# Optimization experiments

Measured on AMD Instinct MI355X. Metric: run time of the kernel, lower is better.

## Reference

```python
import jax, jax.numpy as jnp
import numpy as np

B, C, L, K = 64, 2, 131072, 4


def setup_inputs() -> dict:
    key = jax.random.key(0)
    k1, k2, k3, k4 = jax.random.split(key, 4)
    x = jax.random.normal(k1, (B, C, L), dtype=jnp.float32)
    Bs = 0.5 * jax.random.normal(k2, (B, C, K, 3), dtype=jnp.float32)
    # Build stable denominators: complex-conjugate poles r*exp(+-j*theta), r < 0.95
    # a(z) = 1 - 2 r cos(theta) z^-1 + r^2 z^-2  -> guaranteed-stable IIR cascade.
    r = jax.random.uniform(k3, (B, C, K), minval=0.1, maxval=0.95)
    theta = jax.random.uniform(k4, (B, C, K), minval=0.05, maxval=np.pi - 0.05)
    a1 = -2.0 * r * jnp.cos(theta)
    a2 = r * r
    As = jnp.stack([jnp.ones_like(a1), a1, a2], axis=-1).astype(jnp.float32)
    return {"input_signal": x, "Bs": Bs, "As": As}


def _biquad_cascade(x, b, a):
    # x: [N, L]; b, a: [N, K, 3] with a already normalized (a0 == 1).
    # Serial cascade of K biquads, each in direct form II transposed:
    #   y[n]  = b0*u[n] + s1
    #   s1'   = b1*u[n] - a1*y[n] + s2
    #   s2'   = b2*u[n] - a2*y[n]
    # Exactly the linear recurrence the ssm/lfilter backends compute.
    nK = b.shape[1]
    b0, b1, b2 = b[..., 0], b[..., 1], b[..., 2]  # each [N, K]
    a1, a2 = a[..., 1], a[..., 2]

    def step(carry, xt):
        s1, s2 = carry  # each [N, K]
        u = xt  # [N]
        s1n, s2n = [], []
        for k in range(nK):  # small fixed cascade depth, unrolled
            y = b0[:, k] * u + s1[:, k]
            s1n.append(b1[:, k] * u - a1[:, k] * y + s2[:, k])
            s2n.append(b2[:, k] * u - a2[:, k] * y)
            u = y
        return (jnp.stack(s1n, axis=1), jnp.stack(s2n, axis=1)), u

    N = x.shape[0]
    init = (jnp.zeros((N, nK), x.dtype), jnp.zeros((N, nK), x.dtype))
    _, ys = jax.lax.scan(step, init, x.T)  # scan over time: ys [L, N]
    return ys.T


def reference(input_signal, Bs, As):
    b, c, audio_len = input_signal.shape
    assert Bs.shape[-1] == As.shape[-1] == 3
    # channel broadcasting as in _process_ssm
    if c == 1 and Bs.shape[1] > 1:
        input_signal = jnp.broadcast_to(input_signal, (b, Bs.shape[1], audio_len))
        c = Bs.shape[1]
    elif Bs.shape[1] == 1 and c > 1:
        Bs = jnp.broadcast_to(Bs, (b, c) + Bs.shape[2:])
        As = jnp.broadcast_to(As, (b, c) + As.shape[2:])
    a0 = As[..., :1]
    Bn = (Bs / a0).reshape(b * c, -1, 3)
    An = (As / a0).reshape(b * c, -1, 3)
    x = input_signal.reshape(b * c, audio_len)
    y = _biquad_cascade(x, Bn, An)
    return y.reshape(b, c, audio_len)
```

## Files before the change

kernel.cpp:

```cpp
#include <hip/hip_runtime.h>
#include <math.h>


#define SS   64
#define WMAX 384
#define WMIN 64
#define TT   32
#define TPB  256
#define LSTR 33
#define KB   4
#define NL   8

typedef float vf4 __attribute__((ext_vector_type(4)));

__global__ void iir_prep_kernel(const float* __restrict__ As, int rows,
                                int* __restrict__ wrow, int* __restrict__ perm)
{
    __shared__ int sw[256];
    const int r = threadIdx.x;
    int W = 0;
    if (r < rows) {
        float r2max = 0.f;
#pragma unroll
        for (int k = 0; k < KB; ++k) {
            float a0 = As[(size_t)r * KB * 3 + 3 * k];
            float a2 = As[(size_t)r * KB * 3 + 3 * k + 2] / a0;
            r2max = fmaxf(r2max, a2);
        }
        float rmax = fminf(fmaxf(sqrtf(fmaxf(r2max, 0.f)), 0.20f), 0.955f);
        float Wf = 25.6f / (-logf(rmax));
        W = ((int)ceilf(Wf) + TT - 1) & ~(TT - 1);
        W = min(max(W, WMIN), WMAX);
        wrow[r] = W;
    }
    sw[r] = W;
    __syncthreads();
    if (r < rows) {
        int rank = 0;
        for (int i = 0; i < rows; ++i)
            rank += (sw[i] > W) || (sw[i] == W && i < r);
        perm[rank] = r;
    }
}

__global__ __launch_bounds__(TPB, 4) void iir_chunks_kernel(
    const float* __restrict__ x, const float* __restrict__ Bs,
    const float* __restrict__ As, float* __restrict__ out, int L,
    const int* __restrict__ wrow, const int* __restrict__ perm)
{
    __shared__ float lds[TPB * LSTR];
    const int tid = threadIdx.x;
    const int bpr = (L / SS) / TPB;
    const int row = perm[blockIdx.x / bpr];
    const int chunk0 = (blockIdx.x % bpr) * TPB;
    const int W = wrow[row];

    float b0[KB], b1[KB], b2[KB], na1[KB], na2[KB];
    const float* Bp = Bs + (size_t)row * KB * 3;
    const float* Ap = As + (size_t)row * KB * 3;
#pragma unroll
    for (int k = 0; k < KB; ++k) {
        float inv = 1.0f / Ap[3 * k];
        b0[k]  =  Bp[3 * k]     * inv;
        b1[k]  =  Bp[3 * k + 1] * inv;
        b2[k]  =  Bp[3 * k + 2] * inv;
        na1[k] = -Ap[3 * k + 1] * inv;
        na2[k] = -Ap[3 * k + 2] * inv;
    }

    float s1[KB] = {0.f, 0.f, 0.f, 0.f};
    float s2[KB] = {0.f, 0.f, 0.f, 0.f};

    const float* xrow = x   + (size_t)row * L;
    float*       orow = out + (size_t)row * L;
    float*       myrow = lds + tid * LSTR;

    const int tq = tid >> 3;
    const int p4 = (tid & 7) << 2;
    int off[NL];
    int ldsoff[NL];
#pragma unroll
    for (int l = 0; l < NL; ++l) {
        int j = l * 32 + tq;
        off[l]    = (chunk0 + j) * SS + p4 - W;
        ldsoff[l] = j * LSTR + p4;
    }

    const int NT = (SS + W) / TT;
    const int WT = W / TT;

    float4 rn[NL];
#pragma unroll
    for (int l = 0; l < NL; ++l) {
        int pos = off[l];
        rn[l] = make_float4(0.f, 0.f, 0.f, 0.f);
        if (pos >= 0) rn[l] = *reinterpret_cast<const float4*>(xrow + pos);
    }

#pragma unroll 1
    for (int it = 0; it < NT; ++it) {
        __syncthreads();

#pragma unroll
        for (int l = 0; l < NL; ++l) {
            float* d = lds + ldsoff[l];
            d[0] = rn[l].x; d[1] = rn[l].y; d[2] = rn[l].z; d[3] = rn[l].w;
        }

        if (it + 1 < NT) {
            const int base = (it + 1) * TT;
#pragma unroll
            for (int l = 0; l < NL; ++l) {
                int pos = off[l] + base;
                rn[l] = make_float4(0.f, 0.f, 0.f, 0.f);
                if (pos >= 0) rn[l] = *reinterpret_cast<const float4*>(xrow + pos);
            }
        }

        __syncthreads();

        if (it < WT) {
#pragma unroll
            for (int p = 0; p < TT; ++p) {
                float u = myrow[p];
#pragma unroll
                for (int k = 0; k < KB; ++k) {
                    float yv = fmaf(b0[k], u, s1[k]);
                    s1[k] = fmaf(na1[k], yv, fmaf(b1[k], u, s2[k]));
                    s2[k] = fmaf(na2[k], yv, b2[k] * u);
                    u = yv;
                }
            }
        } else {
#pragma unroll
            for (int p = 0; p < TT; ++p) {
                float u = myrow[p];
#pragma unroll
                for (int k = 0; k < KB; ++k) {
                    float yv = fmaf(b0[k], u, s1[k]);
                    s1[k] = fmaf(na1[k], yv, fmaf(b1[k], u, s2[k]));
                    s2[k] = fmaf(na2[k], yv, b2[k] * u);
                    u = yv;
                }
                myrow[p] = u;
            }
            __syncthreads();

            const int base = it * TT - W;
#pragma unroll
            for (int l = 0; l < NL; ++l) {
                const float* sp = lds + ldsoff[l];
                vf4 v = { sp[0], sp[1], sp[2], sp[3] };
                __builtin_nontemporal_store(
                    v, reinterpret_cast<vf4*>(orow + off[l] + W + base));
            }
        }
    }
}

extern "C" void kernel_launch(void* const* d_in, const int* in_sizes, int n_in,
                              void* d_out, int out_size, void* d_ws, size_t ws_size,
                              hipStream_t stream) {
    const float* x  = (const float*)d_in[0];
    const float* Bs = (const float*)d_in[1];
    const float* As = (const float*)d_in[2];
    float* out = (float*)d_out;

    const int rows = in_sizes[1] / (KB * 3);
    const int L    = in_sizes[0] / rows;
    const int bpr  = (L / SS) / TPB;

    int* wrow = (int*)d_ws;
    int* perm = wrow + rows;

    hipLaunchKernelGGL(iir_prep_kernel, dim3(1), dim3(256), 0, stream,
                       As, rows, wrow, perm);
    hipLaunchKernelGGL(iir_chunks_kernel, dim3(rows * bpr), dim3(TPB), 0, stream,
                       x, Bs, As, out, L, wrow, perm);
}
```

Baseline: 141.2 us.

## Replace warm-up halo recompute with chunk-state pass plus transition-matrix combine

```diff
diff --git a/kernel.cpp b/kernel.cpp
--- a/kernel.cpp
+++ b/kernel.cpp
@@ -10,8 +10,311 @@
 #define LSTR 33
 #define KB   4
 #define NL   8
+#define HALO 6
+#define DSTR 9
 
 typedef float vf4 __attribute__((ext_vector_type(4)));
+
+__global__ void iir_prep2_kernel(const float* __restrict__ Bs,
+                                 const float* __restrict__ As, int rows,
+                                 int* __restrict__ nwrow,
+                                 float* __restrict__ nmat)
+{
+    __shared__ float mat[4][3][64];
+    const int grp  = threadIdx.x >> 6;
+    const int lane = threadIdx.x & 63;
+    const int row  = blockIdx.x * 4 + grp;
+    const bool act = (row < rows);
+
+    float b0[KB], b1[KB], b2[KB], na1[KB], na2[KB];
+    if (act) {
+        const float* Bp = Bs + (size_t)row * KB * 3;
+        const float* Ap = As + (size_t)row * KB * 3;
+#pragma unroll
+        for (int k = 0; k < KB; ++k) {
+            float inv = 1.0f / Ap[3 * k];
+            b0[k]  =  Bp[3 * k]     * inv;
+            b1[k]  =  Bp[3 * k + 1] * inv;
+            b2[k]  =  Bp[3 * k + 2] * inv;
+            na1[k] = -Ap[3 * k + 1] * inv;
+            na2[k] = -Ap[3 * k + 2] * inv;
+        }
+    }
+
+    float* cur = &mat[grp][0][0];
+    float* nxt = &mat[grp][1][0];
+    float* n1  = &mat[grp][2][0];
+
+    if (act && lane < 8) {
+        float s[8];
+#pragma unroll
+        for (int i = 0; i < 8; ++i) s[i] = (i == lane) ? 1.0f : 0.0f;
+        float u = 0.0f;
+#pragma unroll
+        for (int k = 0; k < KB; ++k) {
+            float y  = fmaf(b0[k], u, s[2 * k]);
+            float t1 = fmaf(na1[k], y, fmaf(b1[k], u, s[2 * k + 1]));
+            float t2 = fmaf(na2[k], y, b2[k] * u);
+            s[2 * k] = t1; s[2 * k + 1] = t2; u = y;
+        }
+#pragma unroll
+        for (int i = 0; i < 8; ++i) cur[i * 8 + lane] = s[i];
+    }
+    __syncthreads();
+
+    const int i8 = lane >> 3, j8 = lane & 7;
+
+    for (int t = 0; t < 6; ++t) {
+        float acc = 0.0f;
+        if (act) {
+#pragma unroll
+            for (int m = 0; m < 8; ++m)
+                acc = fmaf(cur[i8 * 8 + m], cur[m * 8 + j8], acc);
+            nxt[lane] = acc;
+        }
+        __syncthreads();
+        float* t0 = cur; cur = nxt; nxt = t0;
+    }
+
+    if (act) {
+        float v = cur[lane];
+        n1[lane] = v;
+        nmat[(size_t)row * 320 + lane] = v;
+    }
+    __syncthreads();
+
+    for (int m = 2; m <= 5; ++m) {
+        float acc = 0.0f;
+        if (act) {
+#pragma unroll
+            for (int q = 0; q < 8; ++q)
+                acc = fmaf(cur[i8 * 8 + q], n1[q * 8 + j8], acc);
+            nxt[lane] = acc;
+            nmat[(size_t)row * 320 + (m - 1) * 64 + lane] = acc;
+        }
+        __syncthreads();
+        float* t0 = cur; cur = nxt; nxt = t0;
+    }
+
+    if (act && lane == 0) {
+        const float* Ap = As + (size_t)row * KB * 3;
+        float r2max = 0.0f;
+#pragma unroll
+        for (int k = 0; k < KB; ++k) {
+            float a0 = Ap[3 * k];
+            float a2 = Ap[3 * k + 2] / a0;
+            r2max = fmaxf(r2max, a2);
+        }
+        float rmax = fminf(fmaxf(sqrtf(fmaxf(r2max, 0.f)), 0.20f), 0.955f);
+        float Wf = 25.6f / (-logf(rmax));
+        int W = ((int)ceilf(Wf) + TT - 1) & ~(TT - 1);
+        W = min(max(W, WMIN), WMAX);
+        nwrow[row] = (W + SS - 1) / SS;
+    }
+}
+
+__global__ __launch_bounds__(TPB, 4) void iir_state_kernel(
+    const float* __restrict__ x, const float* __restrict__ Bs,
+    const float* __restrict__ As, int L, float* __restrict__ dstate)
+{
+    __shared__ float lds[TPB * LSTR];
+    const int tid = threadIdx.x;
+    const int cpr = L / SS;
+    const int bpr = cpr / TPB;
+    const int row = blockIdx.x / bpr;
+    const int chunk0 = (blockIdx.x % bpr) * TPB;
+
+    float b0[KB], b1[KB], b2[KB], na1[KB], na2[KB];
+    const float* Bp = Bs + (size_t)row * KB * 3;
+    const float* Ap = As + (size_t)row * KB * 3;
+#pragma unroll
+    for (int k = 0; k < KB; ++k) {
+        float inv = 1.0f / Ap[3 * k];
+        b0[k]  =  Bp[3 * k]     * inv;
+        b1[k]  =  Bp[3 * k + 1] * inv;
+        b2[k]  =  Bp[3 * k + 2] * inv;
+        na1[k] = -Ap[3 * k + 1] * inv;
+        na2[k] = -Ap[3 * k + 2] * inv;
+    }
+
+    float s1[KB] = {0.f, 0.f, 0.f, 0.f};
+    float s2[KB] = {0.f, 0.f, 0.f, 0.f};
+
+    const float* xrow = x + (size_t)row * L;
+    float* myrow = lds + tid * LSTR;
+
+    const int tq = tid >> 3;
+    const int p4 = (tid & 7) << 2;
+    int off[NL], ldsoff[NL];
+#pragma unroll
+    for (int l = 0; l < NL; ++l) {
+        int j = l * 32 + tq;
+        off[l]    = (chunk0 + j) * SS + p4;
+        ldsoff[l] = j * LSTR + p4;
+    }
+
+    float4 rn[NL];
+#pragma unroll
+    for (int l = 0; l < NL; ++l)
+        rn[l] = *reinterpret_cast<const float4*>(xrow + off[l]);
+
+#pragma unroll
+    for (int it = 0; it < SS / TT; ++it) {
+        __syncthreads();
+#pragma unroll
+        for (int l = 0; l < NL; ++l) {
+            float* d = lds + ldsoff[l];
+            d[0] = rn[l].x; d[1] = rn[l].y; d[2] = rn[l].z; d[3] = rn[l].w;
+        }
+        if (it + 1 < SS / TT) {
+            const int base = (it + 1) * TT;
+#pragma unroll
+            for (int l = 0; l < NL; ++l)
+                rn[l] = *reinterpret_cast<const float4*>(xrow + off[l] + base);
+        }
+        __syncthreads();
+
+#pragma unroll
+        for (int p = 0; p < TT; ++p) {
+            float u = myrow[p];
+#pragma unroll
+            for (int k = 0; k < KB; ++k) {
+                float yv = fmaf(b0[k], u, s1[k]);
+                s1[k] = fmaf(na1[k], yv, fmaf(b1[k], u, s2[k]));
+                s2[k] = fmaf(na2[k], yv, b2[k] * u);
+                u = yv;
+            }
+        }
+    }
+
+    float* dp = dstate + ((size_t)row * cpr + chunk0 + tid) * 8;
+    float4 d0 = make_float4(s1[0], s2[0], s1[1], s2[1]);
+    float4 d1 = make_float4(s1[2], s2[2], s1[3], s2[3]);
+    *reinterpret_cast<float4*>(dp)     = d0;
+    *reinterpret_cast<float4*>(dp + 4) = d1;
+}
+
+__global__ __launch_bounds__(TPB, 4) void iir_out_kernel(
+    const float* __restrict__ x, const float* __restrict__ Bs,
+    const float* __restrict__ As, float* __restrict__ out, int L,
+    const float* __restrict__ dstate, const float* __restrict__ nmat,
+    const int* __restrict__ nwrow)
+{
+    __shared__ float lds[TPB * LSTR];
+    const int tid = threadIdx.x;
+    const int cpr = L / SS;
+    const int bpr = cpr / TPB;
+    const int row = blockIdx.x / bpr;
+    const int chunk0 = (blockIdx.x % bpr) * TPB;
+    const int nW = nwrow[row];
+
+    float b0[KB], b1[KB], b2[KB], na1[KB], na2[KB];
+    const float* Bp = Bs + (size_t)row * KB * 3;
+    const float* Ap = As + (size_t)row * KB * 3;
+#pragma unroll
+    for (int k = 0; k < KB; ++k) {
+        float inv = 1.0f / Ap[3 * k];
+        b0[k]  =  Bp[3 * k]     * inv;
+        b1[k]  =  Bp[3 * k + 1] * inv;
+        b2[k]  =  Bp[3 * k + 2] * inv;
+        na1[k] = -Ap[3 * k + 1] * inv;
+        na2[k] = -Ap[3 * k + 2] * inv;
+    }
+
+    const float* xrow = x   + (size_t)row * L;
+    float*       orow = out + (size_t)row * L;
+    float*       myrow = lds + tid * LSTR;
+
+    const int tq = tid >> 3;
+    const int p4 = (tid & 7) << 2;
+    int off[NL], ldsoff[NL];
+#pragma unroll
+    for (int l = 0; l < NL; ++l) {
+        int j = l * 32 + tq;
+        off[l]    = (chunk0 + j) * SS + p4;
+        ldsoff[l] = j * LSTR + p4;
+    }
+
+    float4 rn[NL];
+#pragma unroll
+    for (int l = 0; l < NL; ++l)
+        rn[l] = *reinterpret_cast<const float4*>(xrow + off[l]);
+
+    float* dl = lds;
+    float* nl = lds + (TPB + HALO) * DSTR;
+    const float* dbase = dstate + ((size_t)row * cpr + chunk0 - HALO) * 8;
+    for (int e = tid; e < (TPB + HALO) * 8; e += TPB) {
+        int c  = e >> 3;
+        int gi = chunk0 - HALO + c;
+        float v = 0.0f;
+        if (gi >= 0) v = dbase[e];
+        dl[c * DSTR + (e & 7)] = v;
+    }
+    for (int e = tid; e < 320; e += TPB) nl[e] = nmat[(size_t)row * 320 + e];
+    __syncthreads();
+
+    float p[8];
+#pragma unroll
+    for (int i = 0; i < 8; ++i) p[i] = dl[(tid + HALO - 1) * DSTR + i];
+#pragma unroll 1
+    for (int m = 2; m <= nW; ++m) {
+        const float* M  = nl + (m - 2) * 64;
+        const float* dd = dl + (tid + HALO - m) * DSTR;
+        float din[8];
+#pragma unroll
+        for (int q = 0; q < 8; ++q) din[q] = dd[q];
+#pragma unroll
+        for (int i = 0; i < 8; ++i) {
+            float a = p[i];
+#pragma unroll
+            for (int q = 0; q < 8; ++q) a = fmaf(M[i * 8 + q], din[q], a);
+            p[i] = a;
+        }
+    }
+    float s1[KB], s2[KB];
+#pragma unroll
+    for (int k = 0; k < KB; ++k) { s1[k] = p[2 * k]; s2[k] = p[2 * k + 1]; }
+
+#pragma unroll
+    for (int it = 0; it < SS / TT; ++it) {
+        __syncthreads();
+#pragma unroll
+        for (int l = 0; l < NL; ++l) {
+            float* d = lds + ldsoff[l];
+            d[0] = rn[l].x; d[1] = rn[l].y; d[2] = rn[l].z; d[3] = rn[l].w;
+        }
+        if (it + 1 < SS / TT) {
+            const int base = (it + 1) * TT;
+#pragma unroll
+            for (int l = 0; l < NL; ++l)
+                rn[l] = *reinterpret_cast<const float4*>(xrow + off[l] + base);
+        }
+        __syncthreads();
+
+#pragma unroll
+        for (int q = 0; q < TT; ++q) {
+            float u = myrow[q];
+#pragma unroll
+            for (int k = 0; k < KB; ++k) {
+                float yv = fmaf(b0[k], u, s1[k]);
+                s1[k] = fmaf(na1[k], yv, fmaf(b1[k], u, s2[k]));
+                s2[k] = fmaf(na2[k], yv, b2[k] * u);
+                u = yv;
+            }
+            myrow[q] = u;
+        }
+        __syncthreads();
+
+        const int base = it * TT;
+#pragma unroll
+        for (int l = 0; l < NL; ++l) {
+            const float* sp = lds + ldsoff[l];
+            vf4 v = { sp[0], sp[1], sp[2], sp[3] };
+            __builtin_nontemporal_store(
+                v, reinterpret_cast<vf4*>(orow + off[l] + base));
+        }
+    }
+}
 
 __global__ void iir_prep_kernel(const float* __restrict__ As, int rows,
                                 int* __restrict__ wrow, int* __restrict__ perm)
@@ -77,8 +380,7 @@
 
     const int tq = tid >> 3;
     const int p4 = (tid & 7) << 2;
-    int off[NL];
-    int ldsoff[NL];
+    int off[NL], ldsoff[NL];
 #pragma unroll
     for (int l = 0; l < NL; ++l) {
         int j = l * 32 + tq;
@@ -100,13 +402,11 @@
 #pragma unroll 1
     for (int it = 0; it < NT; ++it) {
         __syncthreads();
-
 #pragma unroll
         for (int l = 0; l < NL; ++l) {
             float* d = lds + ldsoff[l];
             d[0] = rn[l].x; d[1] = rn[l].y; d[2] = rn[l].z; d[3] = rn[l].w;
         }
-
         if (it + 1 < NT) {
             const int base = (it + 1) * TT;
 #pragma unroll
@@ -116,7 +416,6 @@
                 if (pos >= 0) rn[l] = *reinterpret_cast<const float4*>(xrow + pos);
             }
         }
-
         __syncthreads();
 
         if (it < WT) {
@@ -168,13 +467,27 @@
 
     const int rows = in_sizes[1] / (KB * 3);
     const int L    = in_sizes[0] / rows;
-    const int bpr  = (L / SS) / TPB;
-
-    int* wrow = (int*)d_ws;
-    int* perm = wrow + rows;
-
-    hipLaunchKernelGGL(iir_prep_kernel, dim3(1), dim3(256), 0, stream,
-                       As, rows, wrow, perm);
-    hipLaunchKernelGGL(iir_chunks_kernel, dim3(rows * bpr), dim3(TPB), 0, stream,
-                       x, Bs, As, out, L, wrow, perm);
-}
+    const int cpr  = L / SS;
+    const int bpr  = cpr / TPB;
+
+    float* dstate = (float*)d_ws;
+    float* nmat   = dstate + (size_t)rows * cpr * 8;
+    int*   nwrow  = (int*)(nmat + (size_t)rows * 320);
+    const size_t need = (size_t)((char*)(nwrow + rows) - (char*)d_ws);
+
+    if ((L % SS) == 0 && bpr * TPB == cpr && ws_size >= need) {
+        hipLaunchKernelGGL(iir_prep2_kernel, dim3((rows + 3) / 4), dim3(256), 0,
+                           stream, Bs, As, rows, nwrow, nmat);
+        hipLaunchKernelGGL(iir_state_kernel, dim3(rows * bpr), dim3(TPB), 0,
+                           stream, x, Bs, As, L, dstate);
+        hipLaunchKernelGGL(iir_out_kernel, dim3(rows * bpr), dim3(TPB), 0,
+                           stream, x, Bs, As, out, L, dstate, nmat, nwrow);
+    } else {
+        int* wrow = (int*)d_ws;
+        int* perm = wrow + rows;
+        hipLaunchKernelGGL(iir_prep_kernel, dim3(1), dim3(256), 0, stream,
+                           As, rows, wrow, perm);
+        hipLaunchKernelGGL(iir_chunks_kernel, dim3(rows * bpr), dim3(TPB), 0,
+                           stream, x, Bs, As, out, L, wrow, perm);
+    }
+}
```

New measurement: 133.3 us. 5.6% less time.
